# Optimization experiments

Hardware: AMD Instinct MI355X
Metric: run time of the kernel (lower is better)

The kernel has to match this reference:

```python
import jax, jax.numpy as jnp
import numpy as np

B, K, D, H = 16, 256, 256, 128

def setup_inputs() -> dict:
    key = jax.random.key(0)
    k1, k2, k3 = jax.random.split(key, 3)
    x = jax.random.normal(k1, (B, K, D), dtype=jnp.float32)
    # Linear(2D, H): weight stored as (2D, H) for x @ W convention
    W1 = jax.random.normal(k2, (2 * D, H), dtype=jnp.float32) * (1.0 / np.sqrt(2 * D))
    b1 = jnp.zeros((H,), dtype=jnp.float32)
    W2 = jax.random.normal(k3, (H, D), dtype=jnp.float32) * (1.0 / np.sqrt(H))
    b2 = jnp.zeros((D,), dtype=jnp.float32)
    return {"x": x, "W1": W1, "b1": b1, "W2": W2, "b2": b2}

def reference(x, W1, b1, W2, b2):
    # Original: for each i, concat([x_i broadcast, x_j]) -> Linear -> ReLU -> Linear -> mean_j, + residual.
    # Split the first Linear over the concat: W1 = [W1a; W1b], so
    # pre-act(i,j) = x_i @ W1a + x_j @ W1b + b1  (avoids materializing the concat).
    D_ = x.shape[-1]
    W1a, W1b = W1[:D_], W1[D_:]
    a = jnp.einsum('bkd,dh->bkh', x, W1a)            # B x K x H (query side)
    b = jnp.einsum('bkd,dh->bkh', x, W1b)            # B x K x H (key side)
    h = jax.nn.relu(a[:, :, None, :] + b[:, None, :, :] + b1)  # B x K x K x H
    mh = h.mean(axis=2)                               # mean over j; Linear commutes with mean
    out = jnp.einsum('bkh,hd->bkd', mh, W2) + b2      # B x K x D
    return out + x
```

## Files before the change

### kernel.cpp

```cpp
#include <hip/hip_runtime.h>

typedef __attribute__((ext_vector_type(8))) short bf16x8;
typedef __attribute__((ext_vector_type(4))) float f32x4;
typedef __attribute__((ext_vector_type(2))) float f32x2;

union FragU { uint4 q; bf16x8 h; };

__device__ __forceinline__ unsigned cvt_pk(float lo, float hi) {
  unsigned r;
  asm("v_cvt_pk_bf16_f32 %0, %1, %2" : "=v"(r) : "v"(lo), "v"(hi));
  return r;
}

__global__ __launch_bounds__(1024) void kA(
    const float* __restrict__ x, const float* __restrict__ W1,
    const float* __restrict__ b1, uint4* __restrict__ mf)
{
  __shared__ __align__(16) unsigned short xs[256 * 256];
  __shared__ float As[8][260];
  __shared__ float Cs[8][260];
  __shared__ float PB[8][260];

  const int tid = threadIdx.x, lane = tid & 63, wv = tid >> 6;
  const int b = blockIdx.x, hc = blockIdx.y;
  const int fr = lane & 15, fq = lane >> 4;

#pragma unroll
  for (int i = 0; i < 16; ++i) {
    const int idx = i * 1024 + tid;
    const int row = idx >> 6, u = idx & 63;
    float4 v = *(const float4*)&x[(size_t)(b * 256 + row) * 256 + u * 4];
    uint2 hv = make_uint2(cvt_pk(v.x, v.y), cvt_pk(v.z, v.w));
    *(uint2*)&xs[row * 256 + (u ^ ((row & 7) << 1)) * 4] = hv;
  }

  const float* __restrict__ wp =
      W1 + (size_t)((fr >= 8) ? 256 : 0) * 128 + hc * 8 + (fr & 7);
  FragU afr[8];
#pragma unroll
  for (int c = 0; c < 8; ++c) {
    float v[8];
#pragma unroll
    for (int j = 0; j < 8; ++j) v[j] = wp[(size_t)(c * 32 + fq * 8 + j) * 128];
    afr[c].q = make_uint4(cvt_pk(v[0], v[1]), cvt_pk(v[2], v[3]),
                          cvt_pk(v[4], v[5]), cvt_pk(v[6], v[7]));
  }

  float b1v[4];
#pragma unroll
  for (int g = 0; g < 4; ++g)
    b1v[g] = (fq >= 2) ? b1[hc * 8 + (fq - 2) * 4 + g] : 0.f;

  __syncthreads();

  {
    const int mrow = wv * 16 + fr;
    const int swz = (mrow & 7) << 1;
    f32x4 acc = {0.f, 0.f, 0.f, 0.f};
#pragma unroll
    for (int c = 0; c < 8; ++c) {
      const int pu = (c * 8 + fq * 2) ^ swz;
      bf16x8 bfr = *(const bf16x8*)&xs[mrow * 256 + pu * 4];
      acc = __builtin_amdgcn_mfma_f32_16x16x32_bf16(afr[c].h, bfr, acc, 0, 0, 0);
    }
    if (fq < 2) {
#pragma unroll
      for (int g = 0; g < 4; ++g) As[fq * 4 + g][mrow] = acc[g];
    } else {
#pragma unroll
      for (int g = 0; g < 4; ++g) Cs[(fq - 2) * 4 + g][mrow] = acc[g] + b1v[g];
    }
  }
  __syncthreads();

  const int hp = wv & 7, kh = wv >> 3;
  const float a0 = As[hp][lane],       a1 = As[hp][64 + lane];
  const float a2 = As[hp][128 + lane], a3 = As[hp][192 + lane];

  float sumC = 0.f;
  if (kh == 0) {
    float4 s4 = *(const float4*)&Cs[hp][lane * 4];
    sumC = (s4.x + s4.y) + (s4.z + s4.w);
#pragma unroll
    for (int off = 32; off >= 1; off >>= 1) sumC += __shfl_xor(sumC, off, 64);
  }

  const f32x2 aa0 = {a0, a0}, aa1 = {a1, a1}, aa2 = {a2, a2}, aa3 = {a3, a3};
  float s0l = 0.f, s0h = 0.f, s1l = 0.f, s1h = 0.f;
  float s2l = 0.f, s2h = 0.f, s3l = 0.f, s3h = 0.f;
  const int u0 = kh * 32;

#define PROW(aa, sl, sh)                                                   \
  {                                                                        \
    f32x2 t0, t1;                                                          \
    asm("v_pk_add_f32 %0, %1, %2" : "=v"(t0) : "v"(aa), "v"(c01));         \
    asm("v_pk_add_f32 %0, %1, %2" : "=v"(t1) : "v"(aa), "v"(c23));         \
    sl += __builtin_fabsf(t0.x); sh += __builtin_fabsf(t0.y);              \
    sl += __builtin_fabsf(t1.x); sh += __builtin_fabsf(t1.y);              \
  }

#pragma unroll 8
  for (int u = 0; u < 32; ++u) {
    float4 c4 = *(const float4*)&Cs[hp][(u0 + u) * 4];
    f32x2 c01 = {c4.x, c4.y}, c23 = {c4.z, c4.w};
    PROW(aa0, s0l, s0h)
    PROW(aa1, s1l, s1h)
    PROW(aa2, s2l, s2h)
    PROW(aa3, s3l, s3h)
  }
#undef PROW

  if (kh == 1) {
    PB[hp][lane]       = s0l + s0h;
    PB[hp][64 + lane]  = s1l + s1h;
    PB[hp][128 + lane] = s2l + s2h;
    PB[hp][192 + lane] = s3l + s3h;
  }
  __syncthreads();

  if (kh == 0) {
    As[hp][lane]       = (256.f * a0 + sumC + (s0l + s0h) + PB[hp][lane])       * (1.f / 512.f);
    As[hp][64 + lane]  = (256.f * a1 + sumC + (s1l + s1h) + PB[hp][64 + lane])  * (1.f / 512.f);
    As[hp][128 + lane] = (256.f * a2 + sumC + (s2l + s2h) + PB[hp][128 + lane]) * (1.f / 512.f);
    As[hp][192 + lane] = (256.f * a3 + sumC + (s3l + s3h) + PB[hp][192 + lane]) * (1.f / 512.f);
  }
  __syncthreads();

  if (tid < 256) {
    const int fr2 = tid & 15, T = tid >> 4;
    uint4 o = make_uint4(cvt_pk(As[0][tid], As[1][tid]), cvt_pk(As[2][tid], As[3][tid]),
                         cvt_pk(As[4][tid], As[5][tid]), cvt_pk(As[6][tid], As[7][tid]));
    mf[((size_t)(b * 16 + T) * 4 + (hc >> 2)) * 64 + (hc & 3) * 16 + fr2] = o;
  }
}

__global__ __launch_bounds__(256) void kB(
    const uint4* __restrict__ mf, const float* __restrict__ W2,
    const float* __restrict__ b2, const float* __restrict__ x,
    float* __restrict__ out)
{
  const int tid = threadIdx.x, lane = tid & 63, wu = tid >> 6;
  const int mt = blockIdx.x;
  const int dg = blockIdx.y * 4 + wu;
  const int fr = lane & 15, fq = lane >> 4;

  const float* __restrict__ w2p = W2 + dg * 16 + fr;
  FragU bfr[4];
#pragma unroll
  for (int c = 0; c < 4; ++c) {
    float v[8];
#pragma unroll
    for (int j = 0; j < 8; ++j) v[j] = w2p[(size_t)(c * 32 + fq * 8 + j) * 256];
    bfr[c].q = make_uint4(cvt_pk(v[0], v[1]), cvt_pk(v[2], v[3]),
                          cvt_pk(v[4], v[5]), cvt_pk(v[6], v[7]));
  }

  f32x4 acc = {0.f, 0.f, 0.f, 0.f};
#pragma unroll
  for (int c = 0; c < 4; ++c) {
    FragU a;
    a.q = mf[((size_t)mt * 4 + c) * 64 + lane];
    acc = __builtin_amdgcn_mfma_f32_16x16x32_bf16(a.h, bfr[c].h, acc, 0, 0, 0);
  }

  const int d = dg * 16 + fr;
  const float bv = b2[d];
#pragma unroll
  for (int g = 0; g < 4; ++g) {
    const int m = mt * 16 + fq * 4 + g;
    const size_t o = (size_t)m * 256 + d;
    out[o] = acc[g] + bv + x[o];
  }
}

extern "C" void kernel_launch(void* const* d_in, const int* in_sizes, int n_in,
                              void* d_out, int out_size, void* d_ws, size_t ws_size,
                              hipStream_t stream) {
  const float* x  = (const float*)d_in[0];
  const float* W1 = (const float*)d_in[1];
  const float* b1 = (const float*)d_in[2];
  const float* W2 = (const float*)d_in[3];
  const float* b2 = (const float*)d_in[4];
  float* out = (float*)d_out;

  uint4* mf = (uint4*)d_ws;

  kA<<<dim3(16, 16), 1024, 0, stream>>>(x, W1, b1, mf);
  kB<<<dim3(256, 4), 256, 0, stream>>>(mf, W2, b2, x, out);
}
```

Before: 25.91 us.

## Pre-convert x to bf16 MFMA fragments and split kA into smaller blocks

```diff
diff --git a/kernel.cpp b/kernel.cpp
--- a/kernel.cpp
+++ b/kernel.cpp
@@ -12,68 +12,74 @@
   return r;
 }
 
-__global__ __launch_bounds__(1024) void kA(
-    const float* __restrict__ x, const float* __restrict__ W1,
+__global__ __launch_bounds__(256) void kX(
+    const float* __restrict__ x, uint4* __restrict__ xbf)
+{
+  const int u = blockIdx.x * 256 + threadIdx.x;
+  const int l = u & 63, c = (u >> 6) & 7, t = (u >> 9) & 15, b = u >> 13;
+  const int fr = l & 15, fq = l >> 4;
+  const float* p = x + (size_t)((b * 16 + t) * 16 + fr) * 256 + c * 32 + fq * 8;
+  float4 va = *(const float4*)p;
+  float4 vb = *(const float4*)(p + 4);
+  xbf[u] = make_uint4(cvt_pk(va.x, va.y), cvt_pk(va.z, va.w),
+                      cvt_pk(vb.x, vb.y), cvt_pk(vb.z, vb.w));
+}
+
+__global__ __launch_bounds__(512) void kA(
+    const uint4* __restrict__ xbf, const float* __restrict__ W1,
     const float* __restrict__ b1, uint4* __restrict__ mf)
 {
-  __shared__ __align__(16) unsigned short xs[256 * 256];
-  __shared__ float As[8][260];
-  __shared__ float Cs[8][260];
-  __shared__ float PB[8][260];
+  __shared__ float As[4][260];
+  __shared__ float Cs[4][260];
+  __shared__ float PB[4][260];
 
   const int tid = threadIdx.x, lane = tid & 63, wv = tid >> 6;
-  const int b = blockIdx.x, hc = blockIdx.y;
+  const int b = blockIdx.x, hg = blockIdx.y;
   const int fr = lane & 15, fq = lane >> 4;
 
-#pragma unroll
-  for (int i = 0; i < 16; ++i) {
-    const int idx = i * 1024 + tid;
-    const int row = idx >> 6, u = idx & 63;
-    float4 v = *(const float4*)&x[(size_t)(b * 256 + row) * 256 + u * 4];
-    uint2 hv = make_uint2(cvt_pk(v.x, v.y), cvt_pk(v.z, v.w));
-    *(uint2*)&xs[row * 256 + (u ^ ((row & 7) << 1)) * 4] = hv;
-  }
-
-  const float* __restrict__ wp =
-      W1 + (size_t)((fr >= 8) ? 256 : 0) * 128 + hc * 8 + (fr & 7);
   FragU afr[8];
-#pragma unroll
-  for (int c = 0; c < 8; ++c) {
-    float v[8];
-#pragma unroll
-    for (int j = 0; j < 8; ++j) v[j] = wp[(size_t)(c * 32 + fq * 8 + j) * 128];
-    afr[c].q = make_uint4(cvt_pk(v[0], v[1]), cvt_pk(v[2], v[3]),
-                          cvt_pk(v[4], v[5]), cvt_pk(v[6], v[7]));
+  if (fr < 8) {
+    const float* __restrict__ wp =
+        W1 + (size_t)((fr >= 4) ? 256 : 0) * 128 + hg * 4 + (fr & 3);
+#pragma unroll
+    for (int c = 0; c < 8; ++c) {
+      float v[8];
+#pragma unroll
+      for (int j = 0; j < 8; ++j) v[j] = wp[(size_t)(c * 32 + fq * 8 + j) * 128];
+      afr[c].q = make_uint4(cvt_pk(v[0], v[1]), cvt_pk(v[2], v[3]),
+                            cvt_pk(v[4], v[5]), cvt_pk(v[6], v[7]));
+    }
+  } else {
+#pragma unroll
+    for (int c = 0; c < 8; ++c) afr[c].q = make_uint4(0u, 0u, 0u, 0u);
   }
 
   float b1v[4];
 #pragma unroll
-  for (int g = 0; g < 4; ++g)
-    b1v[g] = (fq >= 2) ? b1[hc * 8 + (fq - 2) * 4 + g] : 0.f;
-
+  for (int g = 0; g < 4; ++g) b1v[g] = b1[hg * 4 + g];
+
+#pragma unroll
+  for (int s = 0; s < 2; ++s) {
+    const int t = wv + s * 8;
+    f32x4 acc = {0.f, 0.f, 0.f, 0.f};
+#pragma unroll
+    for (int c = 0; c < 8; ++c) {
+      FragU bfr;
+      bfr.q = xbf[((size_t)(b * 16 + t) * 8 + c) * 64 + lane];
+      acc = __builtin_amdgcn_mfma_f32_16x16x32_bf16(afr[c].h, bfr.h, acc, 0, 0, 0);
+    }
+    const int m = t * 16 + fr;
+    if (fq == 0) {
+#pragma unroll
+      for (int g = 0; g < 4; ++g) As[g][m] = acc[g];
+    } else if (fq == 1) {
+#pragma unroll
+      for (int g = 0; g < 4; ++g) Cs[g][m] = acc[g] + b1v[g];
+    }
+  }
   __syncthreads();
 
-  {
-    const int mrow = wv * 16 + fr;
-    const int swz = (mrow & 7) << 1;
-    f32x4 acc = {0.f, 0.f, 0.f, 0.f};
-#pragma unroll
-    for (int c = 0; c < 8; ++c) {
-      const int pu = (c * 8 + fq * 2) ^ swz;
-      bf16x8 bfr = *(const bf16x8*)&xs[mrow * 256 + pu * 4];
-      acc = __builtin_amdgcn_mfma_f32_16x16x32_bf16(afr[c].h, bfr, acc, 0, 0, 0);
-    }
-    if (fq < 2) {
-#pragma unroll
-      for (int g = 0; g < 4; ++g) As[fq * 4 + g][mrow] = acc[g];
-    } else {
-#pragma unroll
-      for (int g = 0; g < 4; ++g) Cs[(fq - 2) * 4 + g][mrow] = acc[g] + b1v[g];
-    }
-  }
-  __syncthreads();
-
-  const int hp = wv & 7, kh = wv >> 3;
+  const int hp = wv & 3, kh = wv >> 2;
   const float a0 = As[hp][lane],       a1 = As[hp][64 + lane];
   const float a2 = As[hp][128 + lane], a3 = As[hp][192 + lane];
 
@@ -127,10 +133,13 @@
   __syncthreads();
 
   if (tid < 256) {
-    const int fr2 = tid & 15, T = tid >> 4;
-    uint4 o = make_uint4(cvt_pk(As[0][tid], As[1][tid]), cvt_pk(As[2][tid], As[3][tid]),
-                         cvt_pk(As[4][tid], As[5][tid]), cvt_pk(As[6][tid], As[7][tid]));
-    mf[((size_t)(b * 16 + T) * 4 + (hc >> 2)) * 64 + (hc & 3) * 16 + fr2] = o;
+    const int m = tid, T = m >> 4, fr2 = m & 15;
+    const int cc = hg >> 3;
+    const int fq2 = (hg & 7) >> 1;
+    const size_t unit = ((size_t)(b * 16 + T) * 4 + cc) * 64 + fq2 * 16 + fr2;
+    unsigned* mfd = (unsigned*)mf;
+    uint2 o = make_uint2(cvt_pk(As[0][m], As[1][m]), cvt_pk(As[2][m], As[3][m]));
+    *(uint2*)&mfd[unit * 4 + (hg & 1) * 2] = o;
   }
 }
 
@@ -183,8 +192,11 @@
   const float* b2 = (const float*)d_in[4];
   float* out = (float*)d_out;
 
-  uint4* mf = (uint4*)d_ws;
-
-  kA<<<dim3(16, 16), 1024, 0, stream>>>(x, W1, b1, mf);
+  char* ws = (char*)d_ws;
+  uint4* xbf = (uint4*)ws;
+  uint4* mf  = (uint4*)(ws + (2u << 20));
+
+  kX<<<512, 256, 0, stream>>>(x, xbf);
+  kA<<<dim3(16, 32), 512, 0, stream>>>(xbf, W1, b1, mf);
   kB<<<dim3(256, 4), 256, 0, stream>>>(mf, W2, b2, x, out);
 }
```

New measurement: 29.17 us. +12.6%, slower.
